# Optimization experiments

Measured on AMD Instinct MI355X. Metric: run time of the kernel, lower is better.

The kernel has to match this reference:

```python
import jax, jax.numpy as jnp
import numpy as np

N_FILTERS = 1024
N_HEADS = 8  # hardcoded h=8 in the original einops.rearrange
LN_EPS = 1e-3  # keras LayerNormalization default epsilon


def setup_inputs() -> dict:
    key = jax.random.key(0)
    k1, k2, k3 = jax.random.split(key, 3)
    B, N, C = 4, 2048, N_FILTERS
    x = jax.random.normal(k1, (B, N, C), dtype=jnp.float32)
    ln_gamma = jnp.ones((C,), dtype=jnp.float32)
    ln_beta = jnp.zeros((C,), dtype=jnp.float32)
    w_qkv = jax.random.normal(k2, (C, 3 * C), dtype=jnp.float32) * 0.02
    w_out = jax.random.normal(k3, (C, C), dtype=jnp.float32) * 0.02
    b_out = jnp.zeros((C,), dtype=jnp.float32)
    return {"x": x, "ln_gamma": ln_gamma, "ln_beta": ln_beta,
            "w_qkv": w_qkv, "w_out": w_out, "b_out": b_out}


def reference(x, ln_gamma, ln_beta, w_qkv, w_out, b_out):
    B, N, C = x.shape
    h = N_HEADS
    hd = C // h
    scale = jnp.asarray(float(C) ** (-0.5), dtype=x.dtype)  # note: full C, as in source

    # LayerNorm over last axis (keras default)
    mu = jnp.mean(x, axis=-1, keepdims=True)
    var = jnp.var(x, axis=-1, keepdims=True)
    xn = (x - mu) / jnp.sqrt(var + LN_EPS) * ln_gamma + ln_beta

    # QKV projection (no bias): [B, N, 3C]
    qkv = jnp.einsum('bnc,cd->bnd', xn, w_qkv)
    # rearrange 'b n (qkv h c) -> qkv b h n c'
    qkv = qkv.reshape(B, N, 3, h, hd).transpose(2, 0, 3, 1, 4)
    q, k, v = qkv[0], qkv[1], qkv[2]

    # attention: [B, h, N, N]
    scores = jnp.einsum('bhnc,bhmc->bhnm', q, k) * scale
    attn = jax.nn.softmax(scores, axis=-1)
    out = jnp.einsum('bhnm,bhmc->bhnc', attn, v)
    # 'b h n c -> b n (h c)'
    out = out.transpose(0, 2, 1, 3).reshape(B, N, C)

    out = jnp.einsum('bnc,cd->bnd', out, w_out) + b_out
    return x + out
```

## Files before the change

### kernel.cpp

```cpp
#include <hip/hip_runtime.h>

typedef _Float16 half8 __attribute__((ext_vector_type(8)));
typedef float floatx4 __attribute__((ext_vector_type(4)));

#define BB 4
#define SEQ 2048
#define CHN 1024
#define NH 8
#define HD 128
#define CQ 3072

__device__ __forceinline__ float bf2f(unsigned short b) {
  unsigned int u = ((unsigned int)b) << 16;
  float f; __builtin_memcpy(&f, &u, 4); return f;
}
__device__ __forceinline__ unsigned short f2bf(float f) {
  unsigned int u; __builtin_memcpy(&u, &f, 4);
  u += 0x7fffu + ((u >> 16) & 1u);
  return (unsigned short)(u >> 16);
}
__device__ __forceinline__ void gl_lds16(const _Float16* g, _Float16* l) {
  __builtin_amdgcn_global_load_lds(
      (const __attribute__((address_space(1))) unsigned int*)(g),
      (__attribute__((address_space(3))) unsigned int*)(l), 16, 0, 0);
}

__global__ __launch_bounds__(256) void detect_k(
    const unsigned int* __restrict__ x, int* __restrict__ flag) {
  __shared__ int bad;
  if (threadIdx.x == 0) bad = 0;
  __syncthreads();
  int b = 0;
#pragma unroll
  for (int i = 0; i < 8; ++i) {
    unsigned int w = x[threadIdx.x * 8 + i];
    float v = bf2f((unsigned short)(w & 0xffffu));
    if (!(fabsf(v) < 1e4f)) b = 1;
  }
  if (b) bad = 1;
  __syncthreads();
  if (threadIdx.x == 0) *flag = bad;
}

__global__ __launch_bounds__(256) void transpose_b2h(
    const void* __restrict__ in, _Float16* __restrict__ out, int R, int C,
    const int* __restrict__ flag) {
  __shared__ _Float16 tile[64][66];
  int isf = *flag;
  int ti = blockIdx.y, tj = blockIdx.x, t = threadIdx.x;
  if (isf) {
    const float* inf = (const float*)in;
#pragma unroll
    for (int i = 0; i < 16; ++i) {
      int lin = i * 256 + t;
      int r = lin >> 6, c = lin & 63;
      tile[r][c] = (_Float16)inf[(size_t)(ti * 64 + r) * C + tj * 64 + c];
    }
  } else {
    const unsigned short* inb = (const unsigned short*)in;
#pragma unroll
    for (int i = 0; i < 16; ++i) {
      int lin = i * 256 + t;
      int r = lin >> 6, c = lin & 63;
      tile[r][c] = (_Float16)bf2f(inb[(size_t)(ti * 64 + r) * C + tj * 64 + c]);
    }
  }
  __syncthreads();
#pragma unroll
  for (int i = 0; i < 16; ++i) {
    int lin = i * 256 + t;
    int c = lin >> 6, r = lin & 63;
    out[(size_t)(tj * 64 + c) * R + ti * 64 + r] = tile[r][c];
  }
}

__global__ __launch_bounds__(256) void ln_k(
    const void* __restrict__ xv, const void* __restrict__ gv,
    const void* __restrict__ bv, _Float16* __restrict__ xn,
    const int* __restrict__ flag) {
  int isf = *flag;
  int row = blockIdx.x, t = threadIdx.x;
  float v0, v1, v2, v3;
  if (isf) {
    const float4 f = *reinterpret_cast<const float4*>((const float*)xv + (size_t)row * CHN + t * 4);
    v0 = f.x; v1 = f.y; v2 = f.z; v3 = f.w;
  } else {
    ushort4 u = *reinterpret_cast<const ushort4*>((const unsigned short*)xv + (size_t)row * CHN + t * 4);
    v0 = bf2f(u.x); v1 = bf2f(u.y); v2 = bf2f(u.z); v3 = bf2f(u.w);
  }
  float s = v0 + v1 + v2 + v3;
  float ss = v0 * v0 + v1 * v1 + v2 * v2 + v3 * v3;
#pragma unroll
  for (int off = 32; off >= 1; off >>= 1) {
    s += __shfl_xor(s, off, 64);
    ss += __shfl_xor(ss, off, 64);
  }
  __shared__ float red[8];
  int wave = t >> 6, lane = t & 63;
  if (lane == 0) { red[wave] = s; red[4 + wave] = ss; }
  __syncthreads();
  s = red[0] + red[1] + red[2] + red[3];
  ss = red[4] + red[5] + red[6] + red[7];
  float mu = s * (1.0f / CHN);
  float var = ss * (1.0f / CHN) - mu * mu;
  float rstd = rsqrtf(var + 1e-3f);
  float g0, g1, g2, g3, b0, b1, b2, b3;
  if (isf) {
    const float4 g = *reinterpret_cast<const float4*>((const float*)gv + t * 4);
    const float4 b = *reinterpret_cast<const float4*>((const float*)bv + t * 4);
    g0 = g.x; g1 = g.y; g2 = g.z; g3 = g.w;
    b0 = b.x; b1 = b.y; b2 = b.z; b3 = b.w;
  } else {
    ushort4 g = *reinterpret_cast<const ushort4*>((const unsigned short*)gv + t * 4);
    ushort4 b = *reinterpret_cast<const ushort4*>((const unsigned short*)bv + t * 4);
    g0 = bf2f(g.x); g1 = bf2f(g.y); g2 = bf2f(g.z); g3 = bf2f(g.w);
    b0 = bf2f(b.x); b1 = bf2f(b.y); b2 = bf2f(b.z); b3 = bf2f(b.w);
  }
  _Float16* o = xn + (size_t)row * CHN + t * 4;
  o[0] = (_Float16)((v0 - mu) * rstd * g0 + b0);
  o[1] = (_Float16)((v1 - mu) * rstd * g1 + b1);
  o[2] = (_Float16)((v2 - mu) * rstd * g2 + b2);
  o[3] = (_Float16)((v3 - mu) * rstd * g3 + b3);
}

template <int EPI>
__global__ __launch_bounds__(256, 3) void gemm_k(
    const _Float16* __restrict__ A, const _Float16* __restrict__ Bt,
    int M, int Nn, int K,
    _Float16* __restrict__ outh, void* __restrict__ outv,
    const void* __restrict__ bias, const void* __restrict__ resid,
    const int* __restrict__ flag) {
  __shared__ _Float16 As[128 * 64];
  __shared__ _Float16 Bs[128 * 64];
  int isf = (EPI == 1) ? *flag : 0;
  int t = threadIdx.x;
  int wave = t >> 6, lane = t & 63, quad = lane >> 4, l15 = lane & 15;
  int wm = wave >> 1, wn = wave & 1;
  size_t arow0 = (size_t)blockIdx.y * 128;
  size_t brow0 = (size_t)blockIdx.x * 128;
  int lr = lane >> 3, lc = lane & 7;
  int gc = lc ^ lr;
  const _Float16* Abase = A + (arow0 + wave * 32 + lr) * (size_t)K + gc * 8;
  const _Float16* Bbase = Bt + (brow0 + wave * 32 + lr) * (size_t)K + gc * 8;
  floatx4 acc[4][4] = {};
  int nkt = K >> 6;
  for (int kt = 0; kt < nkt; ++kt) {
#pragma unroll
    for (int i = 0; i < 4; ++i) {
      gl_lds16(Abase + kt * 64 + (size_t)i * 8 * K, As + (wave * 32 + i * 8) * 64);
      gl_lds16(Bbase + kt * 64 + (size_t)i * 8 * K, Bs + (wave * 32 + i * 8) * 64);
    }
    __syncthreads();
#pragma unroll
    for (int ks = 0; ks < 2; ++ks) {
      half8 af[4], bfr[4];
#pragma unroll
      for (int mt = 0; mt < 4; ++mt) {
        int row = wm * 64 + mt * 16 + l15;
        int slot = (ks * 4 + quad) ^ (l15 & 7);
        af[mt] = *reinterpret_cast<const half8*>(As + row * 64 + slot * 8);
      }
#pragma unroll
      for (int nt = 0; nt < 4; ++nt) {
        int row = wn * 64 + nt * 16 + l15;
        int slot = (ks * 4 + quad) ^ (l15 & 7);
        bfr[nt] = *reinterpret_cast<const half8*>(Bs + row * 64 + slot * 8);
      }
#pragma unroll
      for (int mt = 0; mt < 4; ++mt)
#pragma unroll
        for (int nt = 0; nt < 4; ++nt)
          acc[mt][nt] = __builtin_amdgcn_mfma_f32_16x16x32_f16(af[mt], bfr[nt], acc[mt][nt], 0, 0, 0);
    }
    __syncthreads();
  }
#pragma unroll
  for (int mt = 0; mt < 4; ++mt) {
#pragma unroll
    for (int r = 0; r < 4; ++r) {
      size_t row = arow0 + wm * 64 + mt * 16 + quad * 4 + r;
#pragma unroll
      for (int nt = 0; nt < 4; ++nt) {
        size_t col = brow0 + wn * 64 + nt * 16 + l15;
        float v = acc[mt][nt][r];
        if (EPI == 0) {
          outh[row * Nn + col] = (_Float16)v;
        } else {
          if (isf) {
            v += ((const float*)bias)[col] + ((const float*)resid)[row * Nn + col];
            ((float*)outv)[row * Nn + col] = v;
          } else {
            v += bf2f(((const unsigned short*)bias)[col]) +
                 bf2f(((const unsigned short*)resid)[row * Nn + col]);
            ((unsigned short*)outv)[row * Nn + col] = f2bf(v);
          }
        }
      }
    }
  }
}

__global__ __launch_bounds__(256) void vtrans_k(
    const _Float16* __restrict__ qkv, _Float16* __restrict__ vtr) {
  __shared__ _Float16 tile[64][72];
  int t = threadIdx.x;
  int tok0 = blockIdx.x * 64;
  int hd0 = blockIdx.y * 64;
  int bh = blockIdx.z;
  int b = bh >> 3, h = bh & 7;
  const _Float16* src = qkv + (size_t)b * SEQ * CQ + 2 * CHN + h * HD + hd0;
#pragma unroll
  for (int i = 0; i < 2; ++i) {
    int lin = i * 256 + t;
    int r = lin >> 3, c8 = lin & 7;
    *reinterpret_cast<half8*>(&tile[r][c8 * 8]) =
        *reinterpret_cast<const half8*>(src + (size_t)(tok0 + r) * CQ + c8 * 8);
  }
  __syncthreads();
  _Float16* dst = vtr + ((size_t)bh * HD + hd0) * SEQ + tok0;
#pragma unroll
  for (int i = 0; i < 2; ++i) {
    int lin = i * 256 + t;
    int c = lin >> 3, r8 = lin & 7;
    half8 v;
#pragma unroll
    for (int j = 0; j < 8; ++j) v[j] = tile[r8 * 8 + j][c];
    *reinterpret_cast<half8*>(dst + (size_t)c * SEQ + r8 * 8) = v;
  }
}

__global__ __launch_bounds__(256, 2) void attn_k(
    const _Float16* __restrict__ qkv, const _Float16* __restrict__ vtr,
    _Float16* __restrict__ out) {
  __shared__ _Float16 Ks[2][64 * 128];
  __shared__ _Float16 Vs[2][128 * 64];
  __shared__ _Float16 pl[4 * 32 * 64];
  int t = threadIdx.x;
  int wave = t >> 6, lane = t & 63, quad = lane >> 4, l15 = lane & 15;
  int bh = blockIdx.x & 31;
  int qt = blockIdx.x >> 5;
  int b = bh >> 3, h = bh & 7;
  int qbase = qt * 128;
  const _Float16* qp = qkv + (size_t)b * SEQ * CQ + h * HD;
  const _Float16* kp = qp + CHN;
  const _Float16* vtp = vtr + (size_t)bh * HD * SEQ;
  const _Float16 qsc = (_Float16)0.045085299f;
  half8 aq[2][4];
#pragma unroll
  for (int qs = 0; qs < 2; ++qs) {
    const _Float16* qr = qp + (size_t)(qbase + wave * 32 + qs * 16 + l15) * CQ + quad * 8;
#pragma unroll
    for (int c = 0; c < 4; ++c) {
      half8 v = *reinterpret_cast<const half8*>(qr + c * 32);
#pragma unroll
      for (int j = 0; j < 8; ++j) v[j] = v[j] * qsc;
      aq[qs][c] = v;
    }
  }
  float l_p[2][4] = {};
  floatx4 accO[2][8] = {};
  _Float16* pw = pl + wave * (32 * 64);
  int kr = lane >> 4, ks16 = lane & 15;
  int vr = lane >> 3, vs8 = lane & 7;
#pragma unroll
  for (int i = 0; i < 4; ++i) {
    int r = wave * 16 + i * 4 + kr;
    int gcs = ks16 ^ (r & 15);
    gl_lds16(kp + (size_t)r * CQ + gcs * 8, Ks[0] + (wave * 16 + i * 4) * 128);
  }
#pragma unroll
  for (int i = 0; i < 4; ++i) {
    int r = wave * 32 + i * 8 + vr;
    int gcs = vs8 ^ (r & 7);
    gl_lds16(vtp + (size_t)r * SEQ + gcs * 8, Vs[0] + (wave * 32 + i * 8) * 64);
  }
  __syncthreads();
  for (int kt = 0; kt < SEQ / 64; ++kt) {
    if (kt + 1 < SEQ / 64) {
      int kb2 = (kt + 1) * 64;
      _Float16* vdst = Vs[(kt + 1) & 1];
#pragma unroll
      for (int i = 0; i < 4; ++i) {
        int r = wave * 32 + i * 8 + vr;
        int gcs = vs8 ^ (r & 7);
        gl_lds16(vtp + (size_t)r * SEQ + kb2 + gcs * 8, vdst + (wave * 32 + i * 8) * 64);
      }
      const _Float16* kn = kp + (size_t)kb2 * CQ;
      _Float16* kdst = Ks[(kt + 1) & 1];
#pragma unroll
      for (int i = 0; i < 4; ++i) {
        int r = wave * 16 + i * 4 + kr;
        int gcs = ks16 ^ (r & 15);
        gl_lds16(kn + (size_t)r * CQ + gcs * 8, kdst + (wave * 16 + i * 4) * 128);
      }
    }
    const _Float16* kc = Ks[kt & 1];
    floatx4 accS[2][4] = {};
    __builtin_amdgcn_s_setprio(1);
#pragma unroll
    for (int c = 0; c < 4; ++c)
#pragma unroll
      for (int nt = 0; nt < 4; ++nt) {
        int row = nt * 16 + l15;
        half8 bk = *reinterpret_cast<const half8*>(kc + (row * 16 + ((c * 4 + quad) ^ l15)) * 8);
        accS[0][nt] = __builtin_amdgcn_mfma_f32_16x16x32_f16(aq[0][c], bk, accS[0][nt], 0, 0, 0);
        accS[1][nt] = __builtin_amdgcn_mfma_f32_16x16x32_f16(aq[1][c], bk, accS[1][nt], 0, 0, 0);
      }
    __builtin_amdgcn_s_setprio(0);
#pragma unroll
    for (int qs = 0; qs < 2; ++qs)
#pragma unroll
      for (int nt = 0; nt < 4; ++nt)
#pragma unroll
        for (int r = 0; r < 4; ++r) {
          float p = __builtin_amdgcn_exp2f(accS[qs][nt][r]);
          l_p[qs][r] += p;
          int prow = qs * 16 + quad * 4 + r;
          int pcol = nt * 16 + l15;
          pw[prow * 64 + ((((pcol >> 3) ^ (prow & 7)) << 3) | (pcol & 7))] = (_Float16)p;
        }
    asm volatile("" ::: "memory");
    const _Float16* vc = Vs[kt & 1];
    __builtin_amdgcn_s_setprio(1);
#pragma unroll
    for (int c2 = 0; c2 < 2; ++c2) {
      int pslot = (c2 * 4 + quad) ^ (l15 & 7);
      half8 ap0 = *reinterpret_cast<const half8*>(pw + l15 * 64 + pslot * 8);
      half8 ap1 = *reinterpret_cast<const half8*>(pw + (16 + l15) * 64 + pslot * 8);
#pragma unroll
      for (int o = 0; o < 8; ++o) {
        int row = o * 16 + l15;
        half8 bv = *reinterpret_cast<const half8*>(vc + (row * 8 + ((c2 * 4 + quad) ^ (l15 & 7))) * 8);
        accO[0][o] = __builtin_amdgcn_mfma_f32_16x16x32_f16(ap0, bv, accO[0][o], 0, 0, 0);
        accO[1][o] = __builtin_amdgcn_mfma_f32_16x16x32_f16(ap1, bv, accO[1][o], 0, 0, 0);
      }
    }
    __builtin_amdgcn_s_setprio(0);
    __syncthreads();
  }
#pragma unroll
  for (int qs = 0; qs < 2; ++qs)
#pragma unroll
    for (int r = 0; r < 4; ++r) {
      float l = l_p[qs][r];
#pragma unroll
      for (int off = 8; off >= 1; off >>= 1) l += __shfl_xor(l, off, 64);
      float inv = 1.0f / l;
      size_t row = qbase + wave * 32 + qs * 16 + quad * 4 + r;
      _Float16* orow = out + ((size_t)b * SEQ + row) * CHN + h * HD;
#pragma unroll
      for (int o = 0; o < 8; ++o) orow[o * 16 + l15] = (_Float16)(accO[qs][o][r] * inv);
    }
}

extern "C" void kernel_launch(void* const* d_in, const int* in_sizes, int n_in,
                              void* d_out, int out_size, void* d_ws, size_t ws_size,
                              hipStream_t stream) {
  (void)in_sizes; (void)n_in; (void)out_size; (void)ws_size;
  const void* x = d_in[0];
  const void* gam = d_in[1];
  const void* bet = d_in[2];
  const void* wqkv = d_in[3];
  const void* wout = d_in[4];
  const void* bout = d_in[5];
  char* ws = (char*)d_ws;
  _Float16* xn    = (_Float16*)(ws);
  _Float16* vtr   = (_Float16*)(ws);
  _Float16* qkv   = (_Float16*)(ws + (size_t)16777216);
  _Float16* aout  = (_Float16*)(ws + (size_t)67108864);
  _Float16* wqkvT = (_Float16*)(ws + (size_t)83886080);
  _Float16* woutT = (_Float16*)(ws + (size_t)90177536);
  int* flag       = (int*)(ws + (size_t)92274688);

  detect_k<<<1, 256, 0, stream>>>((const unsigned int*)x, flag);
  transpose_b2h<<<dim3(CQ / 64, CHN / 64), 256, 0, stream>>>(wqkv, wqkvT, CHN, CQ, flag);
  transpose_b2h<<<dim3(CHN / 64, CHN / 64), 256, 0, stream>>>(wout, woutT, CHN, CHN, flag);
  ln_k<<<dim3(BB * SEQ), 256, 0, stream>>>(x, gam, bet, xn, flag);
  gemm_k<0><<<dim3(CQ / 128, BB * SEQ / 128), 256, 0, stream>>>(
      xn, wqkvT, BB * SEQ, CQ, CHN, qkv, nullptr, nullptr, nullptr, flag);
  vtrans_k<<<dim3(SEQ / 64, HD / 64, BB * NH), 256, 0, stream>>>(qkv, vtr);
  attn_k<<<dim3(BB * NH * (SEQ / 128)), 256, 0, stream>>>(qkv, vtr, aout);
  gemm_k<1><<<dim3(CHN / 128, BB * SEQ / 128), 256, 0, stream>>>(
      aout, woutT, BB * SEQ, CHN, CHN, nullptr, d_out, bout, x, flag);
}
```

Before: 281.0 us.

## Use 32x32 MFMA with transposed scores and keep P in registers

The attention inner loop switches from 16x16x32 to 32x32x16 MFMA and computes the transposed score tile (K·Q^T), so each lane already holds softmax probabilities in a layout usable as the A operand of the P·V product. Probabilities are packed to fp16 and exchanged between lane halves with v_permlane32_swap rather than written to and read back from LDS, which removes the per-wave P scratch buffer. Row sums become a per-lane scalar reduced with shuffles at the end. The intent is to cut LDS traffic and instruction count, at the cost of a more intricate register layout and a different output write pattern.

```diff
diff --git a/kernel.cpp b/kernel.cpp
--- a/kernel.cpp
+++ b/kernel.cpp
@@ -2,6 +2,7 @@
 
 typedef _Float16 half8 __attribute__((ext_vector_type(8)));
 typedef float floatx4 __attribute__((ext_vector_type(4)));
+typedef float floatx16 __attribute__((ext_vector_type(16)));
 
 #define BB 4
 #define SEQ 2048
@@ -23,6 +24,10 @@
   __builtin_amdgcn_global_load_lds(
       (const __attribute__((address_space(1))) unsigned int*)(g),
       (__attribute__((address_space(3))) unsigned int*)(l), 16, 0, 0);
+}
+__device__ __forceinline__ unsigned int pkf16(float a, float b) {
+  auto p = __builtin_amdgcn_cvt_pkrtz(a, b);
+  unsigned int u; __builtin_memcpy(&u, &p, 4); return u;
 }
 
 __global__ __launch_bounds__(256) void detect_k(
@@ -234,9 +239,9 @@
     _Float16* __restrict__ out) {
   __shared__ _Float16 Ks[2][64 * 128];
   __shared__ _Float16 Vs[2][128 * 64];
-  __shared__ _Float16 pl[4 * 32 * 64];
   int t = threadIdx.x;
-  int wave = t >> 6, lane = t & 63, quad = lane >> 4, l15 = lane & 15;
+  int wave = t >> 6, lane = t & 63;
+  int l31 = lane & 31, hi = lane >> 5;
   int bh = blockIdx.x & 31;
   int qt = blockIdx.x >> 5;
   int b = bh >> 3, h = bh & 7;
@@ -245,21 +250,19 @@
   const _Float16* kp = qp + CHN;
   const _Float16* vtp = vtr + (size_t)bh * HD * SEQ;
   const _Float16 qsc = (_Float16)0.045085299f;
-  half8 aq[2][4];
-#pragma unroll
-  for (int qs = 0; qs < 2; ++qs) {
-    const _Float16* qr = qp + (size_t)(qbase + wave * 32 + qs * 16 + l15) * CQ + quad * 8;
-#pragma unroll
-    for (int c = 0; c < 4; ++c) {
-      half8 v = *reinterpret_cast<const half8*>(qr + c * 32);
+  half8 aq[8];
+  {
+    const _Float16* qr = qp + (size_t)(qbase + wave * 32 + l31) * CQ + hi * 8;
+#pragma unroll
+    for (int c = 0; c < 8; ++c) {
+      half8 v = *reinterpret_cast<const half8*>(qr + c * 16);
 #pragma unroll
       for (int j = 0; j < 8; ++j) v[j] = v[j] * qsc;
-      aq[qs][c] = v;
-    }
-  }
-  float l_p[2][4] = {};
-  floatx4 accO[2][8] = {};
-  _Float16* pw = pl + wave * (32 * 64);
+      aq[c] = v;
+    }
+  }
+  float l_p = 0.0f;
+  floatx16 accO[4] = {};
   int kr = lane >> 4, ks16 = lane & 15;
   int vr = lane >> 3, vs8 = lane & 7;
 #pragma unroll
@@ -295,61 +298,74 @@
       }
     }
     const _Float16* kc = Ks[kt & 1];
-    floatx4 accS[2][4] = {};
+    floatx16 accST[2] = {};
     __builtin_amdgcn_s_setprio(1);
 #pragma unroll
-    for (int c = 0; c < 4; ++c)
-#pragma unroll
-      for (int nt = 0; nt < 4; ++nt) {
-        int row = nt * 16 + l15;
-        half8 bk = *reinterpret_cast<const half8*>(kc + (row * 16 + ((c * 4 + quad) ^ l15)) * 8);
-        accS[0][nt] = __builtin_amdgcn_mfma_f32_16x16x32_f16(aq[0][c], bk, accS[0][nt], 0, 0, 0);
-        accS[1][nt] = __builtin_amdgcn_mfma_f32_16x16x32_f16(aq[1][c], bk, accS[1][nt], 0, 0, 0);
-      }
+    for (int c = 0; c < 8; ++c) {
+#pragma unroll
+      for (int sub = 0; sub < 2; ++sub) {
+        int row = sub * 32 + l31;
+        int chunk = (c * 2 + hi) ^ (row & 15);
+        half8 ak = *reinterpret_cast<const half8*>(kc + row * 128 + chunk * 8);
+        accST[sub] = __builtin_amdgcn_mfma_f32_32x32x16_f16(ak, aq[c], accST[sub], 0, 0, 0);
+      }
+    }
     __builtin_amdgcn_s_setprio(0);
-#pragma unroll
-    for (int qs = 0; qs < 2; ++qs)
-#pragma unroll
-      for (int nt = 0; nt < 4; ++nt)
-#pragma unroll
-        for (int r = 0; r < 4; ++r) {
-          float p = __builtin_amdgcn_exp2f(accS[qs][nt][r]);
-          l_p[qs][r] += p;
-          int prow = qs * 16 + quad * 4 + r;
-          int pcol = nt * 16 + l15;
-          pw[prow * 64 + ((((pcol >> 3) ^ (prow & 7)) << 3) | (pcol & 7))] = (_Float16)p;
-        }
-    asm volatile("" ::: "memory");
+    float p0[16], p1[16];
+#pragma unroll
+    for (int r = 0; r < 16; ++r) p0[r] = __builtin_amdgcn_exp2f(accST[0][r]);
+#pragma unroll
+    for (int r = 0; r < 16; ++r) p1[r] = __builtin_amdgcn_exp2f(accST[1][r]);
+    {
+      float s0 = 0, s1 = 0, s2 = 0, s3 = 0;
+#pragma unroll
+      for (int r = 0; r < 16; r += 4) {
+        s0 += p0[r] + p1[r];
+        s1 += p0[r + 1] + p1[r + 1];
+        s2 += p0[r + 2] + p1[r + 2];
+        s3 += p0[r + 3] + p1[r + 3];
+      }
+      l_p += (s0 + s1) + (s2 + s3);
+    }
     const _Float16* vc = Vs[kt & 1];
     __builtin_amdgcn_s_setprio(1);
 #pragma unroll
-    for (int c2 = 0; c2 < 2; ++c2) {
-      int pslot = (c2 * 4 + quad) ^ (l15 & 7);
-      half8 ap0 = *reinterpret_cast<const half8*>(pw + l15 * 64 + pslot * 8);
-      half8 ap1 = *reinterpret_cast<const half8*>(pw + (16 + l15) * 64 + pslot * 8);
-#pragma unroll
-      for (int o = 0; o < 8; ++o) {
-        int row = o * 16 + l15;
-        half8 bv = *reinterpret_cast<const half8*>(vc + (row * 8 + ((c2 * 4 + quad) ^ (l15 & 7))) * 8);
-        accO[0][o] = __builtin_amdgcn_mfma_f32_16x16x32_f16(ap0, bv, accO[0][o], 0, 0, 0);
-        accO[1][o] = __builtin_amdgcn_mfma_f32_16x16x32_f16(ap1, bv, accO[1][o], 0, 0, 0);
+    for (int s = 0; s < 4; ++s) {
+      const float* pp = (s & 2) ? p1 : p0;
+      int o8 = (s & 1) * 8;
+      unsigned int u0 = pkf16(pp[o8 + 0], pp[o8 + 1]);
+      unsigned int u1 = pkf16(pp[o8 + 2], pp[o8 + 3]);
+      unsigned int w0 = pkf16(pp[o8 + 4], pp[o8 + 5]);
+      unsigned int w1 = pkf16(pp[o8 + 6], pp[o8 + 7]);
+      asm volatile("v_permlane32_swap_b32 %0, %1" : "+v"(u0), "+v"(w0));
+      asm volatile("v_permlane32_swap_b32 %0, %1" : "+v"(u1), "+v"(w1));
+      union { unsigned int w[4]; half8 h; } fr;
+      fr.w[0] = u0; fr.w[1] = u1; fr.w[2] = w0; fr.w[3] = w1;
+#pragma unroll
+      for (int dt = 0; dt < 4; ++dt) {
+        int row = dt * 32 + l31;
+        int chunk = (2 * s + hi) ^ (row & 7);
+        half8 bv = *reinterpret_cast<const half8*>(vc + row * 64 + chunk * 8);
+        accO[dt] = __builtin_amdgcn_mfma_f32_32x32x16_f16(fr.h, bv, accO[dt], 0, 0, 0);
       }
     }
     __builtin_amdgcn_s_setprio(0);
     __syncthreads();
   }
-#pragma unroll
-  for (int qs = 0; qs < 2; ++qs)
-#pragma unroll
-    for (int r = 0; r < 4; ++r) {
-      float l = l_p[qs][r];
-#pragma unroll
-      for (int off = 8; off >= 1; off >>= 1) l += __shfl_xor(l, off, 64);
-      float inv = 1.0f / l;
-      size_t row = qbase + wave * 32 + qs * 16 + quad * 4 + r;
-      _Float16* orow = out + ((size_t)b * SEQ + row) * CHN + h * HD;
-#pragma unroll
-      for (int o = 0; o < 8; ++o) orow[o * 16 + l15] = (_Float16)(accO[qs][o][r] * inv);
+  l_p += __shfl_xor(l_p, 32, 64);
+  float inv[16];
+#pragma unroll
+  for (int r = 0; r < 16; ++r) {
+    int qrow = (r & 3) + 8 * (r >> 2) + 4 * hi;
+    inv[r] = 1.0f / __shfl(l_p, qrow, 64);
+  }
+  _Float16* obase = out + ((size_t)b * SEQ + qbase + wave * 32) * CHN + h * HD;
+#pragma unroll
+  for (int dt = 0; dt < 4; ++dt)
+#pragma unroll
+    for (int r = 0; r < 16; ++r) {
+      int qrow = (r & 3) + 8 * (r >> 2) + 4 * hi;
+      obase[(size_t)qrow * CHN + dt * 32 + l31] = (_Float16)(accO[dt][r] * inv[r]);
     }
 }
 
```

Result: slower. 295.0 us (+5.0%).
